# Kernel tuning notes

Hardware: AMD Instinct MI355X
Metric: run time of the kernel (lower is better)

Reference implementation:

```python
import jax, jax.numpy as jnp
import numpy as np

W, H, RADIUS = 800, 600, 3
HW = H * W


def setup_inputs() -> dict:
    key = jax.random.key(0)
    ks = jax.random.split(key, 6)
    N, K = 100000, 16
    # sample points so they project inside the 800x600 frame with positive depth
    xy = jax.random.uniform(ks[0], (N, 2), minval=-1.5, maxval=1.5)
    z = jax.random.uniform(ks[1], (N, 1), minval=2.0, maxval=6.0)
    xyz = jnp.concatenate([xy, z], axis=-1)
    rotation = jax.random.normal(ks[2], (N, 4))
    scaling = jax.random.uniform(ks[3], (N, 3))
    opacity = jax.random.uniform(ks[4], (N, 1)) * 0.8
    features = jax.random.normal(ks[5], (N, K, 3)) * 0.3
    camera_intrinsics = jnp.array([[500.0, 0.0, 400.0],
                                   [0.0, 500.0, 300.0],
                                   [0.0, 0.0, 1.0]], dtype=jnp.float32)
    camera_extrinsics = jnp.eye(4, dtype=jnp.float32)
    return dict(xyz=xyz, rotation=rotation, scaling=scaling, opacity=opacity,
                features=features, camera_intrinsics=camera_intrinsics,
                camera_extrinsics=camera_extrinsics)


def _render(xyz, rotation, scaling, opacity, features, camera_intrinsics, camera_extrinsics):
    N = xyz.shape[0]
    dt = xyz.dtype
    # world -> camera (extrinsics inverted, as in the torch code)
    xyz_h = jnp.concatenate([xyz, jnp.ones((N, 1), dt)], axis=-1)  # [N,4]
    T_inv = jnp.linalg.inv(camera_extrinsics)
    xyz_cam = (xyz_h @ T_inv.T)[:, :3]
    # camera -> screen
    scr = xyz_cam @ camera_intrinsics.T
    pxy = scr[:, :2] / scr[:, 2:3]
    depths = xyz_cam[:, 2]
    valid = ((pxy[:, 0] >= 0) & (pxy[:, 0] < W) &
             (pxy[:, 1] >= 0) & (pxy[:, 1] < H) & (depths > 0))
    # int() in python truncates; valid coords are >=0 so trunc == floor
    xi = pxy[:, 0].astype(jnp.int32)
    yi = pxy[:, 1].astype(jnp.int32)
    colors = features[:, 0, :]  # only SH band 0 is used
    # back-to-front: descending depth over all points (invalid ones are no-ops)
    order = jnp.argsort(-depths)
    # fixed 7x7 gaussian stamp: weight = exp(-(dx^2+dy^2)/2)
    d = jnp.arange(-RADIUS, RADIUS + 1)
    dyg, dxg = jnp.meshgrid(d, d, indexing='ij')
    dxs = dxg.reshape(-1)
    dys = dyg.reshape(-1)
    wts = jnp.exp(-(dxs.astype(dt) ** 2 + dys.astype(dt) ** 2) / 2.0)  # [49]

    xs = (xi[order], yi[order], depths[order], opacity[order, 0], colors[order], valid[order])

    def step(carry, pt):
        img, amap, dmap = carry  # img [3,HW+1]; amap,dmap [HW+1] (last slot = dump)
        x, y, dep, op, col, v = pt
        pxs = x + dxs
        pys = y + dys
        inb = v & (pxs >= 0) & (pxs < W) & (pys >= 0) & (pys < H)
        idx = jnp.where(inb, pys * W + pxs, HW)  # OOB/invalid -> dump slot
        a = op * wts  # [49]
        old_img = img[:, idx]                       # [3,49]
        img = img.at[:, idx].set(old_img * (1 - a) + col[:, None] * a)
        oa = amap[idx]
        amap = amap.at[idx].set(oa + a * (1 - oa))
        od = dmap[idx]
        dmap = dmap.at[idx].set(jnp.where((od == 0) | (dep < od), dep, od))
        return (img, amap, dmap), None

    # background color is (0,0,0)
    img0 = jnp.zeros((3, HW + 1), dt)
    a0 = jnp.zeros((HW + 1,), dt)
    d0 = jnp.zeros((HW + 1,), dt)
    (img, amap, dmap), _ = jax.lax.scan(step, (img0, a0, d0), xs)
    image = img[:, :HW].reshape(3, H, W)
    depth = dmap[:HW].reshape(1, H, W)
    alpha = amap[:HW].reshape(1, H, W)
    return image, depth, alpha


def reference(xyz, rotation, scaling, opacity, features, camera_intrinsics, camera_extrinsics):
    return _render(xyz, rotation, scaling, opacity, features,
                   camera_intrinsics, camera_extrinsics)
```

## Files before the change

kernel.cpp:

```cpp
#include <hip/hip_runtime.h>

typedef unsigned long long u64;

#define WIDTH   800
#define HEIGHT  600
#define HWPX    (WIDTH*HEIGHT)
#define RAD     3
#define TILE    8
#define TXN     100
#define TYN     75
#define NTILES  (TXN*TYN)
#define KSUB    4
#define SUBCAP  96
#define TCAP    (KSUB*SUBCAP)
#define RCAP    256

struct alignas(16) Entry {
    u64   key;
    int   xy;
    float op;
    float r, g, b;
    float pad;
};

__global__ void project_bin_kernel(const float* __restrict__ xyz,
                                   const float* __restrict__ opacity,
                                   const float* __restrict__ features,
                                   const float* __restrict__ K,
                                   const float* __restrict__ ext,
                                   int* __restrict__ tileCount,
                                   Entry* __restrict__ entries, int N) {
    __shared__ double tinv[16];
    if (threadIdx.x == 0) {
        double A[4][8];
        for (int i = 0; i < 4; ++i)
            for (int j = 0; j < 4; ++j) { A[i][j] = (double)ext[i*4+j]; A[i][j+4] = (i == j) ? 1.0 : 0.0; }
        for (int c = 0; c < 4; ++c) {
            int p = c; double mx = fabs(A[c][c]);
            for (int r = c+1; r < 4; ++r) { double v = fabs(A[r][c]); if (v > mx) { mx = v; p = r; } }
            if (p != c) for (int j = 0; j < 8; ++j) { double t = A[c][j]; A[c][j] = A[p][j]; A[p][j] = t; }
            double piv = A[c][c];
            for (int j = 0; j < 8; ++j) A[c][j] /= piv;
            for (int r = 0; r < 4; ++r) {
                if (r == c) continue;
                double f = A[r][c];
                for (int j = 0; j < 8; ++j) A[r][j] -= f * A[c][j];
            }
        }
        for (int i = 0; i < 4; ++i)
            for (int j = 0; j < 4; ++j) tinv[i*4+j] = A[i][j+4];
    }
    __syncthreads();

    int i = blockIdx.x * blockDim.x + threadIdx.x;
    if (i >= N) return;

    float op = opacity[i];
    float fr = features[i*48+0], fg = features[i*48+1], fb = features[i*48+2];

    double x = (double)xyz[3*i], y = (double)xyz[3*i+1], z = (double)xyz[3*i+2];
    double cam[3];
#pragma unroll
    for (int j = 0; j < 3; ++j)
        cam[j] = x*tinv[4*j+0] + y*tinv[4*j+1] + z*tinv[4*j+2] + tinv[4*j+3];
    double s0 = cam[0]*(double)K[0] + cam[1]*(double)K[1] + cam[2]*(double)K[2];
    double s1 = cam[0]*(double)K[3] + cam[1]*(double)K[4] + cam[2]*(double)K[5];
    double s2 = cam[0]*(double)K[6] + cam[1]*(double)K[7] + cam[2]*(double)K[8];
    double px = s0 / s2, py = s1 / s2;
    double dep = cam[2];
    bool valid = (px >= 0.0) && (px < (double)WIDTH) && (py >= 0.0) && (py < (double)HEIGHT) && (dep > 0.0);
    if (!valid) return;
    int xi = (int)px, yi = (int)py;

    unsigned db = __float_as_uint((float)dep);
    Entry e;
    e.key = ((u64)(~db) << 32) | (unsigned)i;
    e.xy  = xi | (yi << 16);
    e.op  = op;
    e.r = fr; e.g = fg; e.b = fb;
    e.pad = 0.f;

    int sub = i & (KSUB - 1);

    int x0t = max(xi-RAD, 0) >> 3, x1t = min(xi+RAD, WIDTH-1)  >> 3;
    int y0t = max(yi-RAD, 0) >> 3, y1t = min(yi+RAD, HEIGHT-1) >> 3;
    bool hx = (x1t != x0t), hy = (y1t != y0t);
    int t00 = y0t*TXN + x0t;
    int t01 = t00 + 1;
    int t10 = t00 + TXN;
    int t11 = t10 + 1;

    int p00 = atomicAdd(&tileCount[(t00*KSUB + sub) << 4], 1);
    int p01 = hx        ? atomicAdd(&tileCount[(t01*KSUB + sub) << 4], 1) : SUBCAP;
    int p10 = hy        ? atomicAdd(&tileCount[(t10*KSUB + sub) << 4], 1) : SUBCAP;
    int p11 = (hx && hy)? atomicAdd(&tileCount[(t11*KSUB + sub) << 4], 1) : SUBCAP;

    size_t sb = (size_t)sub * SUBCAP;
    if (p00 < SUBCAP) entries[(size_t)t00*TCAP + sb + p00] = e;
    if (p01 < SUBCAP) entries[(size_t)t01*TCAP + sb + p01] = e;
    if (p10 < SUBCAP) entries[(size_t)t10*TCAP + sb + p10] = e;
    if (p11 < SUBCAP) entries[(size_t)t11*TCAP + sb + p11] = e;
}

__global__ __launch_bounds__(256, 8) void render_kernel(
        const int* __restrict__ tileCount,
        const Entry* __restrict__ entries,
        float* __restrict__ out) {
    __shared__ alignas(16) u64 kbuf[RCAP];
    __shared__ u64    s_mask[RCAP];
    __shared__ float  s_w[49];
    __shared__ int2   s_eop[RCAP];
    __shared__ float4 s_rgbd[RCAP];
    __shared__ float4 r_c[256];
    __shared__ float2 r_ad[256];

    int tile = blockIdx.x;
    int tid  = threadIdx.x;
    int lane = tid & 63, wid = tid >> 6;
    size_t start = (size_t)tile * TCAP;
    int tx0 = (tile % TXN) * TILE;
    int ty0 = (tile / TXN) * TILE;

    int c0 = min(tileCount[(tile*KSUB + 0) << 4], SUBCAP);
    int c1 = min(tileCount[(tile*KSUB + 1) << 4], SUBCAP);
    int c2 = min(tileCount[(tile*KSUB + 2) << 4], SUBCAP);
    int c3 = min(tileCount[(tile*KSUB + 3) << 4], SUBCAP);
    int o1 = c0, o2 = c0 + c1, o3 = c0 + c1 + c2;
    int cnt = o3 + c3;
    if (cnt > RCAP) cnt = RCAP;

    if (tid < 49) {
        int dx = tid % 7 - 3, dy = tid / 7 - 3;
        s_w[tid] = (float)exp(-0.5 * (double)(dx*dx + dy*dy));
    }

    u64 key = ~0ull;
    Entry e;
    float dep = 0.f;
    if (tid < cnt) {
        int s, pos;
        if (tid < o1)      { s = 0; pos = tid; }
        else if (tid < o2) { s = 1; pos = tid - o1; }
        else if (tid < o3) { s = 2; pos = tid - o2; }
        else               { s = 3; pos = tid - o3; }
        e = entries[start + (size_t)s * SUBCAP + pos];
        key = e.key;
        dep = __uint_as_float(~(unsigned)(key >> 32));
    }
    kbuf[tid] = key;
    __syncthreads();

    if (tid < cnt) {
        int rank = 0;
        int cr2 = (cnt + 1) & ~1;
        const ulonglong2* kb2 = (const ulonglong2*)kbuf;
        for (int j = 0; j < cr2; j += 2) {
            ulonglong2 kk = kb2[j >> 1];
            rank += (kk.x < key) + (kk.y < key);
        }
        int dxc = (e.xy & 0xFFFF) - tx0;
        int dyc = (e.xy >> 16)    - ty0;
        int sx = dxc - 3, sy = dyc - 3;
        unsigned rm = (sx >= 0) ? ((0x7Fu << sx) & 0xFFu) : (0x7Fu >> (-sx));
        unsigned ym = (sy >= 0) ? ((0x7Fu << sy) & 0xFFu) : (0x7Fu >> (-sy));
        u64 msk = 0;
#pragma unroll
        for (int r = 0; r < 8; ++r)
            msk |= (u64)((ym >> r) & 1u ? rm : 0u) << (8 * r);
        s_mask[rank] = msk;
        s_eop[rank]  = make_int2((3 - dyc) * 7 + (3 - dxc), __float_as_int(e.op));
        s_rgbd[rank] = make_float4(e.r, e.g, e.b, dep);
    }
    __syncthreads();

    int seg = (cnt + 3) >> 2;
    int sA = wid * seg, sB = min(sA + seg, cnt);
    int m = sB - sA; if (m < 0) m = 0;
    int laneterm = (lane >> 3) * 7 + (lane & 7);

    float T = 1.f, Sr = 0.f, Sg = 0.f, Sb = 0.f, Aa = 0.f, Dm = 0.f;
    for (int k2 = 0; k2 < m; ++k2) {
        int q = sA + k2;
        u64 msk = s_mask[q];
        if ((msk >> lane) & 1ull) {
            int2 eo = s_eop[q];
            float4 cd = s_rgbd[q];
            float w  = s_w[laneterm + eo.x];
            float a  = __int_as_float(eo.y) * w;
            float ia = 1.f - a;
            Sr = Sr * ia + cd.x * a;
            Sg = Sg * ia + cd.y * a;
            Sb = Sb * ia + cd.z * a;
            T *= ia;
            Aa = Aa + a * (1.f - Aa);
            float d = cd.w;
            Dm = (Dm == 0.f || d < Dm) ? d : Dm;
        }
    }

    r_c[tid]  = make_float4(T, Sr, Sg, Sb);
    r_ad[tid] = make_float2(Aa, Dm);
    __syncthreads();

    if (wid == 0) {
        float cr = 0.f, cg = 0.f, cb = 0.f, al = 0.f, dm = 0.f;
#pragma unroll
        for (int w = 0; w < 4; ++w) {
            int q = w * 64 + lane;
            float4 c = r_c[q];
            float2 ad = r_ad[q];
            cr = cr * c.x + c.y;
            cg = cg * c.x + c.z;
            cb = cb * c.x + c.w;
            al = al + ad.x * (1.f - al);
            float d = ad.y;
            if (d != 0.f && (dm == 0.f || d < dm)) dm = d;
        }
        int px = tx0 + (lane & 7);
        int py = ty0 + (lane >> 3);
        int pix = py * WIDTH + px;
        out[pix]          = cr;
        out[HWPX + pix]   = cg;
        out[2*HWPX + pix] = cb;
        out[3*HWPX + pix] = dm;
        out[4*HWPX + pix] = al;
    }
}

extern "C" void kernel_launch(void* const* d_in, const int* in_sizes, int n_in,
                              void* d_out, int out_size, void* d_ws, size_t ws_size,
                              hipStream_t stream) {
    const float* xyz      = (const float*)d_in[0];
    const float* opacity  = (const float*)d_in[3];
    const float* features = (const float*)d_in[4];
    const float* K        = (const float*)d_in[5];
    const float* ext      = (const float*)d_in[6];
    int N = in_sizes[0] / 3;

    char* ws = (char*)d_ws;
    size_t off = 0;
    int* tileCount = (int*)(ws + off);
    off += (size_t)NTILES * KSUB * 16 * sizeof(int);
    off = (off + 127) & ~(size_t)127;
    Entry* entries = (Entry*)(ws + off);
    off += (size_t)NTILES * TCAP * sizeof(Entry);

    hipMemsetAsync(tileCount, 0, (size_t)NTILES * KSUB * 16 * sizeof(int), stream);
    int blocks = (N + 255) / 256;
    project_bin_kernel<<<blocks, 256, 0, stream>>>(xyz, opacity, features, K, ext,
                                                   tileCount, entries, N);
    render_kernel<<<NTILES, 256, 0, stream>>>(tileCount, entries, (float*)d_out);
}
```

Before: 57.69 us.

## Split per-tile entries into key lists plus per-point payload array

Result: no change. 58.13 us (+0.8%).

```diff
diff --git a/kernel.cpp b/kernel.cpp
--- a/kernel.cpp
+++ b/kernel.cpp
@@ -15,13 +15,7 @@
 #define TCAP    (KSUB*SUBCAP)
 #define RCAP    256
 
-struct alignas(16) Entry {
-    u64   key;
-    int   xy;
-    float op;
-    float r, g, b;
-    float pad;
-};
+struct alignas(16) PD { int xy; float op, r, g; float b; int pad[3]; };
 
 __global__ void project_bin_kernel(const float* __restrict__ xyz,
                                    const float* __restrict__ opacity,
@@ -29,7 +23,8 @@
                                    const float* __restrict__ K,
                                    const float* __restrict__ ext,
                                    int* __restrict__ tileCount,
-                                   Entry* __restrict__ entries, int N) {
+                                   u64* __restrict__ keys,
+                                   PD* __restrict__ pd, int N) {
     __shared__ double tinv[16];
     if (threadIdx.x == 0) {
         double A[4][8];
@@ -72,13 +67,14 @@
     if (!valid) return;
     int xi = (int)px, yi = (int)py;
 
+    PD p;
+    p.xy = xi | (yi << 16);
+    p.op = op; p.r = fr; p.g = fg; p.b = fb;
+    p.pad[0] = p.pad[1] = p.pad[2] = 0;
+    pd[i] = p;
+
     unsigned db = __float_as_uint((float)dep);
-    Entry e;
-    e.key = ((u64)(~db) << 32) | (unsigned)i;
-    e.xy  = xi | (yi << 16);
-    e.op  = op;
-    e.r = fr; e.g = fg; e.b = fb;
-    e.pad = 0.f;
+    u64 key = ((u64)(~db) << 32) | (unsigned)i;
 
     int sub = i & (KSUB - 1);
 
@@ -96,15 +92,16 @@
     int p11 = (hx && hy)? atomicAdd(&tileCount[(t11*KSUB + sub) << 4], 1) : SUBCAP;
 
     size_t sb = (size_t)sub * SUBCAP;
-    if (p00 < SUBCAP) entries[(size_t)t00*TCAP + sb + p00] = e;
-    if (p01 < SUBCAP) entries[(size_t)t01*TCAP + sb + p01] = e;
-    if (p10 < SUBCAP) entries[(size_t)t10*TCAP + sb + p10] = e;
-    if (p11 < SUBCAP) entries[(size_t)t11*TCAP + sb + p11] = e;
+    if (p00 < SUBCAP) keys[(size_t)t00*TCAP + sb + p00] = key;
+    if (p01 < SUBCAP) keys[(size_t)t01*TCAP + sb + p01] = key;
+    if (p10 < SUBCAP) keys[(size_t)t10*TCAP + sb + p10] = key;
+    if (p11 < SUBCAP) keys[(size_t)t11*TCAP + sb + p11] = key;
 }
 
 __global__ __launch_bounds__(256, 8) void render_kernel(
         const int* __restrict__ tileCount,
-        const Entry* __restrict__ entries,
+        const u64* __restrict__ keys,
+        const PD* __restrict__ pd,
         float* __restrict__ out) {
     __shared__ alignas(16) u64 kbuf[RCAP];
     __shared__ u64    s_mask[RCAP];
@@ -135,7 +132,7 @@
     }
 
     u64 key = ~0ull;
-    Entry e;
+    PD p;
     float dep = 0.f;
     if (tid < cnt) {
         int s, pos;
@@ -143,8 +140,8 @@
         else if (tid < o2) { s = 1; pos = tid - o1; }
         else if (tid < o3) { s = 2; pos = tid - o2; }
         else               { s = 3; pos = tid - o3; }
-        e = entries[start + (size_t)s * SUBCAP + pos];
-        key = e.key;
+        key = keys[start + (size_t)s * SUBCAP + pos];
+        p = pd[(unsigned)(key & 0xFFFFFFFFull)];
         dep = __uint_as_float(~(unsigned)(key >> 32));
     }
     kbuf[tid] = key;
@@ -158,8 +155,8 @@
             ulonglong2 kk = kb2[j >> 1];
             rank += (kk.x < key) + (kk.y < key);
         }
-        int dxc = (e.xy & 0xFFFF) - tx0;
-        int dyc = (e.xy >> 16)    - ty0;
+        int dxc = (p.xy & 0xFFFF) - tx0;
+        int dyc = (p.xy >> 16)    - ty0;
         int sx = dxc - 3, sy = dyc - 3;
         unsigned rm = (sx >= 0) ? ((0x7Fu << sx) & 0xFFu) : (0x7Fu >> (-sx));
         unsigned ym = (sy >= 0) ? ((0x7Fu << sy) & 0xFFu) : (0x7Fu >> (-sy));
@@ -168,8 +165,8 @@
         for (int r = 0; r < 8; ++r)
             msk |= (u64)((ym >> r) & 1u ? rm : 0u) << (8 * r);
         s_mask[rank] = msk;
-        s_eop[rank]  = make_int2((3 - dyc) * 7 + (3 - dxc), __float_as_int(e.op));
-        s_rgbd[rank] = make_float4(e.r, e.g, e.b, dep);
+        s_eop[rank]  = make_int2((3 - dyc) * 7 + (3 - dxc), __float_as_int(p.op));
+        s_rgbd[rank] = make_float4(p.r, p.g, p.b, dep);
     }
     __syncthreads();
 
@@ -242,12 +239,15 @@
     int* tileCount = (int*)(ws + off);
     off += (size_t)NTILES * KSUB * 16 * sizeof(int);
     off = (off + 127) & ~(size_t)127;
-    Entry* entries = (Entry*)(ws + off);
-    off += (size_t)NTILES * TCAP * sizeof(Entry);
+    PD* pd = (PD*)(ws + off);
+    off += (size_t)N * sizeof(PD);
+    off = (off + 127) & ~(size_t)127;
+    u64* keys = (u64*)(ws + off);
+    off += (size_t)NTILES * TCAP * sizeof(u64);
 
     hipMemsetAsync(tileCount, 0, (size_t)NTILES * KSUB * 16 * sizeof(int), stream);
     int blocks = (N + 255) / 256;
     project_bin_kernel<<<blocks, 256, 0, stream>>>(xyz, opacity, features, K, ext,
-                                                   tileCount, entries, N);
-    render_kernel<<<NTILES, 256, 0, stream>>>(tileCount, entries, (float*)d_out);
+                                                   tileCount, keys, pd, N);
+    render_kernel<<<NTILES, 256, 0, stream>>>(tileCount, keys, pd, (float*)d_out);
 }
```

## Bin each point to its home tile only and gather from 3x3 neighbours

Applied to the files above, without the earlier changes.

Result: no change. 56.64 us (-1.8%).

```diff
diff --git a/kernel.cpp b/kernel.cpp
--- a/kernel.cpp
+++ b/kernel.cpp
@@ -10,18 +10,9 @@
 #define TXN     100
 #define TYN     75
 #define NTILES  (TXN*TYN)
-#define KSUB    4
-#define SUBCAP  96
-#define TCAP    (KSUB*SUBCAP)
+#define CAP     128
 #define RCAP    256
 
-struct alignas(16) Entry {
-    u64   key;
-    int   xy;
-    float op;
-    float r, g, b;
-    float pad;
-};
 
 __global__ void project_bin_kernel(const float* __restrict__ xyz,
                                    const float* __restrict__ opacity,
@@ -29,7 +20,7 @@
                                    const float* __restrict__ K,
                                    const float* __restrict__ ext,
                                    int* __restrict__ tileCount,
-                                   Entry* __restrict__ entries, int N) {
+                                   u64* __restrict__ entries, int N) {
     __shared__ double tinv[16];
     if (threadIdx.x == 0) {
         double A[4][8];
@@ -73,40 +64,28 @@
     int xi = (int)px, yi = (int)py;
 
     unsigned db = __float_as_uint((float)dep);
-    Entry e;
-    e.key = ((u64)(~db) << 32) | (unsigned)i;
-    e.xy  = xi | (yi << 16);
-    e.op  = op;
-    e.r = fr; e.g = fg; e.b = fb;
-    e.pad = 0.f;
-
-    int sub = i & (KSUB - 1);
-
-    int x0t = max(xi-RAD, 0) >> 3, x1t = min(xi+RAD, WIDTH-1)  >> 3;
-    int y0t = max(yi-RAD, 0) >> 3, y1t = min(yi+RAD, HEIGHT-1) >> 3;
-    bool hx = (x1t != x0t), hy = (y1t != y0t);
-    int t00 = y0t*TXN + x0t;
-    int t01 = t00 + 1;
-    int t10 = t00 + TXN;
-    int t11 = t10 + 1;
-
-    int p00 = atomicAdd(&tileCount[(t00*KSUB + sub) << 4], 1);
-    int p01 = hx        ? atomicAdd(&tileCount[(t01*KSUB + sub) << 4], 1) : SUBCAP;
-    int p10 = hy        ? atomicAdd(&tileCount[(t10*KSUB + sub) << 4], 1) : SUBCAP;
-    int p11 = (hx && hy)? atomicAdd(&tileCount[(t11*KSUB + sub) << 4], 1) : SUBCAP;
-
-    size_t sb = (size_t)sub * SUBCAP;
-    if (p00 < SUBCAP) entries[(size_t)t00*TCAP + sb + p00] = e;
-    if (p01 < SUBCAP) entries[(size_t)t01*TCAP + sb + p01] = e;
-    if (p10 < SUBCAP) entries[(size_t)t10*TCAP + sb + p10] = e;
-    if (p11 < SUBCAP) entries[(size_t)t11*TCAP + sb + p11] = e;
+    u64 key  = ((u64)(~db) << 32) | (unsigned)i;
+    u64 xyop = (u64)(unsigned)(xi | (yi << 16)) | ((u64)__float_as_uint(op) << 32);
+
+    int t = (yi >> 3) * TXN + (xi >> 3);
+    int pos = atomicAdd(&tileCount[t << 4], 1);
+    if (pos < CAP) {
+        size_t slot = (size_t)t * CAP + pos;
+        ulonglong2* e2 = (ulonglong2*)entries;
+        e2[slot*2]   = make_ulonglong2(key, xyop);
+        float4 hi = make_float4(fr, fg, fb, 0.f);
+        e2[slot*2+1] = *(ulonglong2*)&hi;
+    }
 }
 
 __global__ __launch_bounds__(256, 8) void render_kernel(
         const int* __restrict__ tileCount,
-        const Entry* __restrict__ entries,
+        const u64* __restrict__ entries,
         float* __restrict__ out) {
     __shared__ alignas(16) u64 kbuf[RCAP];
+    __shared__ int2   s_cxyop[RCAP];
+    __shared__ int    s_src[RCAP];
+    __shared__ int    s_cnt;
     __shared__ u64    s_mask[RCAP];
     __shared__ float  s_w[49];
     __shared__ int2   s_eop[RCAP];
@@ -117,40 +96,58 @@
     int tile = blockIdx.x;
     int tid  = threadIdx.x;
     int lane = tid & 63, wid = tid >> 6;
-    size_t start = (size_t)tile * TCAP;
-    int tx0 = (tile % TXN) * TILE;
-    int ty0 = (tile / TXN) * TILE;
-
-    int c0 = min(tileCount[(tile*KSUB + 0) << 4], SUBCAP);
-    int c1 = min(tileCount[(tile*KSUB + 1) << 4], SUBCAP);
-    int c2 = min(tileCount[(tile*KSUB + 2) << 4], SUBCAP);
-    int c3 = min(tileCount[(tile*KSUB + 3) << 4], SUBCAP);
-    int o1 = c0, o2 = c0 + c1, o3 = c0 + c1 + c2;
-    int cnt = o3 + c3;
-    if (cnt > RCAP) cnt = RCAP;
-
+    int txT = tile % TXN, tyT = tile / TXN;
+    int tx0 = txT * TILE, ty0 = tyT * TILE;
+
+    int nb[9], pre[10];
+    pre[0] = 0;
+#pragma unroll
+    for (int q = 0; q < 9; ++q) {
+        int nx = txT + (q % 3) - 1, ny = tyT + (q / 3) - 1;
+        bool ok = ((unsigned)nx < TXN) && ((unsigned)ny < TYN);
+        int t = ok ? ny * TXN + nx : 0;
+        nb[q] = t;
+        int c = ok ? min(tileCount[t << 4], CAP) : 0;
+        pre[q+1] = pre[q] + c;
+    }
+    int total = pre[9];
+
+    if (tid == 0) s_cnt = 0;
+    kbuf[tid] = ~0ull;
     if (tid < 49) {
         int dx = tid % 7 - 3, dy = tid / 7 - 3;
         s_w[tid] = (float)exp(-0.5 * (double)(dx*dx + dy*dy));
     }
-
-    u64 key = ~0ull;
-    Entry e;
-    float dep = 0.f;
+    __syncthreads();
+
+    const ulonglong2* e2 = (const ulonglong2*)entries;
+    for (int c = tid; c < total; c += 256) {
+        int src = 0;
+#pragma unroll
+        for (int q = 0; q < 9; ++q)
+            if (c >= pre[q] && c < pre[q+1]) src = nb[q] * CAP + (c - pre[q]);
+        ulonglong2 lo = e2[(size_t)src * 2];
+        int xy  = (int)(unsigned)(lo.y & 0xFFFFFFFFull);
+        int dxc = (xy & 0xFFFF) - tx0;
+        int dyc = (xy >> 16)    - ty0;
+        if ((unsigned)(dxc + RAD) <= 13u && (unsigned)(dyc + RAD) <= 13u) {
+            int pos = atomicAdd(&s_cnt, 1);
+            if (pos < RCAP) {
+                kbuf[pos]    = lo.x;
+                s_cxyop[pos] = make_int2(xy, (int)(lo.y >> 32));
+                s_src[pos]   = src;
+            }
+        }
+    }
+    __syncthreads();
+    int cnt = min(s_cnt, RCAP);
+
     if (tid < cnt) {
-        int s, pos;
-        if (tid < o1)      { s = 0; pos = tid; }
-        else if (tid < o2) { s = 1; pos = tid - o1; }
-        else if (tid < o3) { s = 2; pos = tid - o2; }
-        else               { s = 3; pos = tid - o3; }
-        e = entries[start + (size_t)s * SUBCAP + pos];
-        key = e.key;
-        dep = __uint_as_float(~(unsigned)(key >> 32));
-    }
-    kbuf[tid] = key;
-    __syncthreads();
-
-    if (tid < cnt) {
+        u64 key = kbuf[tid];
+        int2 xo = s_cxyop[tid];
+        float4 hi = *(const float4*)(e2 + (size_t)s_src[tid] * 2 + 1);
+        float dep = __uint_as_float(~(unsigned)(key >> 32));
+
         int rank = 0;
         int cr2 = (cnt + 1) & ~1;
         const ulonglong2* kb2 = (const ulonglong2*)kbuf;
@@ -158,8 +155,8 @@
             ulonglong2 kk = kb2[j >> 1];
             rank += (kk.x < key) + (kk.y < key);
         }
-        int dxc = (e.xy & 0xFFFF) - tx0;
-        int dyc = (e.xy >> 16)    - ty0;
+        int dxc = (xo.x & 0xFFFF) - tx0;
+        int dyc = (xo.x >> 16)    - ty0;
         int sx = dxc - 3, sy = dyc - 3;
         unsigned rm = (sx >= 0) ? ((0x7Fu << sx) & 0xFFu) : (0x7Fu >> (-sx));
         unsigned ym = (sy >= 0) ? ((0x7Fu << sy) & 0xFFu) : (0x7Fu >> (-sy));
@@ -168,8 +165,8 @@
         for (int r = 0; r < 8; ++r)
             msk |= (u64)((ym >> r) & 1u ? rm : 0u) << (8 * r);
         s_mask[rank] = msk;
-        s_eop[rank]  = make_int2((3 - dyc) * 7 + (3 - dxc), __float_as_int(e.op));
-        s_rgbd[rank] = make_float4(e.r, e.g, e.b, dep);
+        s_eop[rank]  = make_int2((3 - dyc) * 7 + (3 - dxc), xo.y);
+        s_rgbd[rank] = make_float4(hi.x, hi.y, hi.z, dep);
     }
     __syncthreads();
 
@@ -240,12 +237,12 @@
     char* ws = (char*)d_ws;
     size_t off = 0;
     int* tileCount = (int*)(ws + off);
-    off += (size_t)NTILES * KSUB * 16 * sizeof(int);
+    off += (size_t)NTILES * 16 * sizeof(int);
     off = (off + 127) & ~(size_t)127;
-    Entry* entries = (Entry*)(ws + off);
-    off += (size_t)NTILES * TCAP * sizeof(Entry);
-
-    hipMemsetAsync(tileCount, 0, (size_t)NTILES * KSUB * 16 * sizeof(int), stream);
+    u64* entries = (u64*)(ws + off);
+    off += (size_t)NTILES * CAP * 32;
+
+    hipMemsetAsync(tileCount, 0, (size_t)NTILES * 16 * sizeof(int), stream);
     int blocks = (N + 255) / 256;
     project_bin_kernel<<<blocks, 256, 0, stream>>>(xyz, opacity, features, K, ext,
                                                    tileCount, entries, N);
```
